# Kernel optimization log

Hardware: AMD Instinct MI355X
Metric: run time of the kernel (lower is better)

Reference implementation:

```python
import jax, jax.numpy as jnp
import numpy as np
import math

N_HEAD = 12

def alibi_slopes(h):
    x = (2 ** 8) ** (1.0 / h)
    return jnp.array([1.0 / x ** (i + 1) for i in range(h)], dtype=jnp.float32)

def setup_inputs() -> dict:
    key = jax.random.key(0)
    k0, k1, k2 = jax.random.split(key, 3)
    B, T, C = 4, 2048, 576
    x = jax.random.normal(k0, (B, T, C), dtype=jnp.float32)
    w_qkv = jax.random.normal(k1, (3 * C, C), dtype=jnp.float32) * 0.02
    w_proj = jax.random.normal(k2, (C, C), dtype=jnp.float32) * 0.02
    return {"x": x, "w_qkv": w_qkv, "w_proj": w_proj}

def reference(x, w_qkv, w_proj):
    B, T, C = x.shape
    H = N_HEAD
    D = C // H
    qkv = x @ w_qkv.T  # [B,T,3C]
    q, k, v = jnp.split(qkv, 3, axis=2)
    q = q.reshape(B, T, H, D).transpose(0, 2, 1, 3)  # [B,H,T,D]
    k = k.reshape(B, T, H, D).transpose(0, 2, 1, 3)
    v = v.reshape(B, T, H, D).transpose(0, 2, 1, 3)
    # value residual with v1=None: v = 0.5*v + 0.5*v = v (faithful no-op)
    scale = 1.0 / math.sqrt(D)
    att = jnp.einsum('bhid,bhjd->bhij', q, k) * scale  # [B,H,T,T]
    # ALiBi bias as written: (col - row).clamp(min=0) * slope (zero on causal part)
    col = jnp.arange(T, dtype=jnp.float32)[None, :]
    row = jnp.arange(T, dtype=jnp.float32)[:, None]
    bias = jnp.maximum(col - row, 0.0)[None, :, :] * alibi_slopes(H)[:, None, None]  # [H,T,T]
    att = att + bias[None]
    causal = (jnp.arange(T)[None, :] <= jnp.arange(T)[:, None])  # [T,T] lower-tri
    att = jnp.where(causal[None, None], att, -jnp.inf)
    att = jax.nn.softmax(att, axis=-1)
    y = jnp.einsum('bhij,bhjd->bhid', att, v)  # [B,H,T,D]
    y = y.transpose(0, 2, 1, 3).reshape(B, T, C)
    return y @ w_proj.T
```

## Files before the change

### kernel.cpp

```cpp
#include <hip/hip_runtime.h>
#include <math.h>

#define Bn 4
#define Tn 2048
#define Cn 576
#define Hn 12
#define Dn 48
#define Mn (Bn*Tn)

#define QSCALE (1.4426950408889634f * 0.14433756729740643f)

typedef short  short8  __attribute__((ext_vector_type(8)));
typedef float  floatx4 __attribute__((ext_vector_type(4)));
typedef unsigned short ushort_t;
typedef unsigned short ushort8_t __attribute__((ext_vector_type(8)));

static __device__ __forceinline__ unsigned short f2bf(float f) {
    union { float f; unsigned int u; } v; v.f = f;
    unsigned int r = v.u + 0x7FFFu + ((v.u >> 16) & 1u);
    return (unsigned short)(r >> 16);
}

static __device__ __forceinline__ unsigned int pack_trunc(float a, float b) {
    union { float f; unsigned int u; } ua, ub; ua.f = a; ub.f = b;
    return (ua.u >> 16) | (ub.u & 0xFFFF0000u);
}

static __device__ __forceinline__ void gload16(void* lds, const void* g) {
    __builtin_amdgcn_global_load_lds(
        (const __attribute__((address_space(1))) void*)g,
        (__attribute__((address_space(3))) void*)lds, 16, 0, 0);
}

__global__ __launch_bounds__(256)
void cast3(const float* __restrict__ a, ushort_t* __restrict__ oa, int na4,
           const float* __restrict__ b, ushort_t* __restrict__ ob, int nb4,
           const float* __restrict__ c, ushort_t* __restrict__ oc, int nc4)
{
    int i = blockIdx.x * 256 + threadIdx.x;
    const float* src; ushort_t* dst; int idx;
    if (i < na4)                  { src = a; dst = oa; idx = i; }
    else if (i < na4 + nb4)       { src = b; dst = ob; idx = i - na4; }
    else if (i < na4 + nb4 + nc4) { src = c; dst = oc; idx = i - na4 - nb4; }
    else return;
    float4 v = ((const float4*)src)[idx];
    ushort4 o;
    o.x = f2bf(v.x); o.y = f2bf(v.y); o.z = f2bf(v.z); o.w = f2bf(v.w);
    ((ushort4*)dst)[idx] = o;
}

template<int MODE, int MTILE>
__global__ __launch_bounds__(256)
void gemm_mfma(const ushort_t* __restrict__ A, const ushort_t* __restrict__ W,
               ushort_t* __restrict__ outb, float* __restrict__ outf)
{
    constexpr int SA   = MTILE / 16;
    constexpr int NSEG = SA + 4;
    constexpr int PW   = NSEG / 4;
    constexpr int MF   = MTILE / 64;
    constexpr int NB   = (MODE == 0) ? 27 : 9;
    __shared__ __align__(16) ushort_t Ls[2][NSEG][512];

    const int tid  = threadIdx.x;
    const int wave = tid >> 6;
    const int lane = tid & 63;
    const int m    = lane & 15;
    const int g    = lane >> 4;
    const int bid  = blockIdx.x;
    const int xcd  = bid & 7;
    const int slot = bid >> 3;
    const int n0   = (slot % NB) * 64;
    const int m0   = (xcd + 8 * (slot / NB)) * MTILE;

    floatx4 acc[MF][4];
    #pragma unroll
    for (int i = 0; i < MF; ++i)
        #pragma unroll
        for (int j = 0; j < 4; ++j)
            acc[i][j] = (floatx4){0.f, 0.f, 0.f, 0.f};

    const char* gp[PW];
    int         si[PW];
    #pragma unroll
    for (int i = 0; i < PW; ++i) {
        int s = wave + i * 4;
        si[i] = s;
        gp[i] = (s < SA)
            ? (const char*)(A + (size_t)(m0 + s * 16 + m) * Cn + g * 8)
            : (const char*)(W + (size_t)(n0 + (s - SA) * 16 + m) * Cn + g * 8);
    }

    #pragma unroll
    for (int i = 0; i < PW; ++i) { gload16(&Ls[0][si[i]][0], gp[i]); gp[i] += 64; }
    __syncthreads();

    int buf = 0;
    for (int k0 = 0; k0 < Cn; k0 += 32) {
        if (k0 + 32 < Cn) {
            #pragma unroll
            for (int i = 0; i < PW; ++i) { gload16(&Ls[buf ^ 1][si[i]][0], gp[i]); gp[i] += 64; }
        }
        short8 bf4[4];
        #pragma unroll
        for (int j = 0; j < 4; ++j) bf4[j] = *(const short8*)&Ls[buf][SA + j][lane * 8];
        #pragma unroll
        for (int i = 0; i < MF; ++i) {
            short8 af = *(const short8*)&Ls[buf][wave * MF + i][lane * 8];
            #pragma unroll
            for (int j = 0; j < 4; ++j)
                acc[i][j] = __builtin_amdgcn_mfma_f32_16x16x32_bf16(af, bf4[j], acc[i][j], 0, 0, 0);
        }
        __syncthreads();
        buf ^= 1;
    }

    const size_t per = (size_t)Bn * Hn * Tn * Dn;
    if (MODE == 0) {
        const int which = n0 / Cn;
        const int nb    = n0 - which * Cn;
        const int b     = m0 >> 11;
        const int t0g   = m0 & 2047;
        ushort_t* Lc = (ushort_t*)&Ls[0][0][0];
        if (which == 2) {
            constexpr int RS = MTILE + 8;
            #pragma unroll
            for (int i = 0; i < MF; ++i)
                #pragma unroll
                for (int j = 0; j < 4; ++j) {
                    ushort4 pk;
                    pk.x = f2bf(acc[i][j][0]); pk.y = f2bf(acc[i][j][1]);
                    pk.z = f2bf(acc[i][j][2]); pk.w = f2bf(acc[i][j][3]);
                    *(ushort4*)&Lc[(j * 16 + m) * RS + wave * (MTILE / 4) + i * 16 + g * 4] = pk;
                }
            __syncthreads();
            constexpr int CPC = MTILE / 8;
            constexpr int NIT = 64 * CPC / 256;
            #pragma unroll
            for (int it = 0; it < NIT; ++it) {
                int c    = tid + it * 256;
                int col  = c / CPC;
                int rowc = (c - col * CPC) * 8;
                int n    = nb + col;
                int h    = n / 48;
                int d    = n - h * 48;
                ushort_t* dst = outb + 2 * per
                    + (((size_t)(b * Hn + h) * Dn + d) * Tn) + t0g + rowc;
                *(ushort8_t*)dst = *(const ushort8_t*)&Lc[col * RS + rowc];
            }
        } else {
            const float sc = (which == 0) ? QSCALE : 1.0f;
            #pragma unroll
            for (int i = 0; i < MF; ++i)
                #pragma unroll
                for (int j = 0; j < 4; ++j)
                    #pragma unroll
                    for (int r = 0; r < 4; ++r)
                        Lc[(wave * (MTILE / 4) + i * 16 + g * 4 + r) * 80 + j * 16 + m] =
                            f2bf(acc[i][j][r] * sc);
            __syncthreads();
            constexpr int NIT = MTILE * 8 / 256;
            #pragma unroll
            for (int it = 0; it < NIT; ++it) {
                int c   = tid + it * 256;
                int row = c >> 3;
                int c8  = (c & 7) * 8;
                int n   = nb + c8;
                int h   = n / 48;
                int d   = n - h * 48;
                ushort_t* dst = outb + (size_t)which * per
                    + (((size_t)(b * Hn + h) * Tn + t0g + row) * Dn) + d;
                *(ushort8_t*)dst = *(const ushort8_t*)&Lc[row * 80 + c8];
            }
        }
    } else {
        #pragma unroll
        for (int i = 0; i < MF; ++i) {
            #pragma unroll
            for (int r = 0; r < 4; ++r) {
                int mrow = m0 + wave * (MTILE / 4) + i * 16 + g * 4 + r;
                #pragma unroll
                for (int j = 0; j < 4; ++j)
                    outf[(size_t)mrow * Cn + n0 + j * 16 + m] = acc[i][j][r];
            }
        }
    }
}

__global__ __launch_bounds__(512, 6)
void attn_mfma(const ushort_t* __restrict__ Q, const ushort_t* __restrict__ K,
               const ushort_t* __restrict__ V, ushort_t* __restrict__ Y,
               const ushort_t* __restrict__ zb)
{
    __shared__ __align__(16) ushort_t QPs[16][512];
    __shared__ __align__(16) ushort_t Ks[2][8][512];
    __shared__ __align__(16) ushort_t Vs[2][6][512];

    const int id   = blockIdx.x;
    const int kk   = id / 48;
    const int bh   = id - kk * 48;
    const int QT   = (kk & 1) ? (kk >> 1) : (15 - (kk >> 1));
    const int tid  = threadIdx.x;
    const int wave = tid >> 6;
    const int lane = tid & 63;
    const int m    = lane & 15;
    const int g    = lane >> 4;
    const int q0   = QT * 128;
    const int nkt  = 2 * QT + 2;

    const ushort_t* Qp = Q + (size_t)bh * Tn * Dn;
    const ushort_t* Kp = K + (size_t)bh * Tn * Dn;
    const ushort_t* Vp = V + (size_t)bh * Dn * Tn;

    {
        const char* qrp = (const char*)(Qp + (size_t)(q0 + wave * 16 + m) * Dn);
        gload16(&QPs[wave * 2 + 0][0], qrp + g * 16);
        gload16(&QPs[wave * 2 + 1][0], (g < 2) ? (qrp + 64 + g * 16) : (const char*)zb);
    }

    const bool  kpad = ((wave & 1) == 1) && (g >= 2);
    const char* kptr = kpad ? (const char*)zb
        : (const char*)(Kp + (size_t)((wave >> 1) * 16 + m) * Dn) + (wave & 1) * 64 + g * 16;
    const int   kadv = kpad ? 0 : 64 * Dn * 2;
    const char* vptr = (const char*)(Vp + (size_t)((wave >> 1) * 16 + m) * Tn)
                       + (wave & 1) * 64 + g * 16;
    const int   vadv = 64 * 2;

    gload16(&Ks[0][wave][0], kptr); kptr += kadv;
    if (wave < 6) { gload16(&Vs[0][wave][0], vptr); vptr += vadv; }
    __syncthreads();

    short8 bq[2];
    bq[0] = *(const short8*)&QPs[wave * 2 + 0][lane * 8];
    bq[1] = *(const short8*)&QPs[wave * 2 + 1][lane * 8];

    floatx4 acc[3];
    #pragma unroll
    for (int t = 0; t < 3; ++t) acc[t] = (floatx4){0.f, 0.f, 0.f, 0.f};
    float l_tot = 0.f;
    const int qrow  = q0 + wave * 16 + m;
    const int qwmin = q0 + wave * 16;
    const int qwmax = qwmin + 15;

    for (int jt = 0; jt < nkt; ++jt) {
        const int cur = jt & 1;
        const int j0  = jt * 64;
        if (jt + 1 < nkt) {
            gload16(&Ks[cur ^ 1][wave][0], kptr); kptr += kadv;
            if (wave < 6) { gload16(&Vs[cur ^ 1][wave][0], vptr); vptr += vadv; }
        }

        if (j0 <= qwmax) {
            floatx4 s[4];
            #pragma unroll
            for (int t = 0; t < 4; ++t) {
                s[t] = (floatx4){0.f, 0.f, 0.f, 0.f};
                #pragma unroll
                for (int kc = 0; kc < 2; ++kc) {
                    short8 ak = *(const short8*)&Ks[cur][t * 2 + kc][lane * 8];
                    s[t] = __builtin_amdgcn_mfma_f32_16x16x32_bf16(ak, bq[kc], s[t], 0, 0, 0);
                }
            }

            float p[4][4];
            float lsum = 0.f;
            if (j0 + 63 > qwmin) {
                #pragma unroll
                for (int t = 0; t < 4; ++t)
                    #pragma unroll
                    for (int r = 0; r < 4; ++r) {
                        int j = j0 + t * 16 + g * 4 + r;
                        float v = (j <= qrow) ? s[t][r] : -1e30f;
                        float e = __builtin_amdgcn_exp2f(v);
                        p[t][r] = e; lsum += e;
                    }
            } else {
                #pragma unroll
                for (int t = 0; t < 4; ++t)
                    #pragma unroll
                    for (int r = 0; r < 4; ++r) {
                        float e = __builtin_amdgcn_exp2f(s[t][r]);
                        p[t][r] = e; lsum += e;
                    }
            }
            lsum += __shfl_xor(lsum, 16);
            lsum += __shfl_xor(lsum, 32);
            l_tot += lsum;

            #pragma unroll
            for (int t = 0; t < 4; ++t) {
                uint2 w2;
                w2.x = pack_trunc(p[t][0], p[t][1]);
                w2.y = pack_trunc(p[t][2], p[t][3]);
                *(uint2*)&QPs[wave * 2 + (t >> 1)]
                             [(2 * (t & 1) + (g >> 1)) * 128 + m * 8 + (g & 1) * 4] = w2;
            }
            asm volatile("s_waitcnt lgkmcnt(0)" ::: "memory");

            #pragma unroll
            for (int kc = 0; kc < 2; ++kc) {
                short8 bp = *(const short8*)&QPs[wave * 2 + kc][lane * 8];
                #pragma unroll
                for (int t = 0; t < 3; ++t) {
                    short8 av = *(const short8*)&Vs[cur][t * 2 + kc][lane * 8];
                    acc[t] = __builtin_amdgcn_mfma_f32_16x16x32_bf16(av, bp, acc[t], 0, 0, 0);
                }
            }
        }

        __syncthreads();
    }

    const float inv = 1.0f / l_tot;
    const int b = bh / Hn;
    const int h = bh - b * Hn;
    ushort_t* yp = Y + ((size_t)(b * Tn + qrow)) * Cn + h * Dn;
    #pragma unroll
    for (int t = 0; t < 3; ++t) {
        ushort4 o;
        o.x = f2bf(acc[t][0] * inv);
        o.y = f2bf(acc[t][1] * inv);
        o.z = f2bf(acc[t][2] * inv);
        o.w = f2bf(acc[t][3] * inv);
        *(ushort4*)&yp[t * 16 + g * 4] = o;
    }
}

extern "C" void kernel_launch(void* const* d_in, const int* in_sizes, int n_in,
                              void* d_out, int out_size, void* d_ws, size_t ws_size,
                              hipStream_t stream)
{
    const float* x      = (const float*)d_in[0];
    const float* w_qkv  = (const float*)d_in[1];
    const float* w_proj = (const float*)d_in[2];
    float* out = (float*)d_out;

    const size_t per = (size_t)Bn * Hn * Tn * Dn;

    ushort_t* xb  = (ushort_t*)d_ws;
    ushort_t* wqb = xb  + (size_t)Mn * Cn;
    ushort_t* wpb = wqb + (size_t)3 * Cn * Cn;
    ushort_t* qkv = wpb + (size_t)Cn * Cn;
    ushort_t* yb  = qkv + 3 * per;
    ushort_t* zb  = yb  + (size_t)Mn * Cn;

    hipMemsetAsync(zb, 0, 256, stream);

    const int na4 = Mn * Cn / 4, nb4 = 3 * Cn * Cn / 4, nc4 = Cn * Cn / 4;
    cast3<<<dim3((na4 + nb4 + nc4 + 255) / 256), dim3(256), 0, stream>>>(
        x, xb, na4, w_qkv, wqb, nb4, w_proj, wpb, nc4);

    gemm_mfma<0, 256><<<dim3((Mn / 256) * 27), dim3(256), 0, stream>>>(xb, wqb, qkv, nullptr);

    attn_mfma<<<dim3((Tn / 128) * Bn * Hn), dim3(512), 0, stream>>>(
        qkv, qkv + per, qkv + 2 * per, yb, zb);

    gemm_mfma<1, 128><<<dim3((Mn / 128) * 9), dim3(256), 0, stream>>>(yb, wpb, nullptr, out);
}
```

Before: 185.8 us.

## Deepen GEMM K-loop pipeline to four LDS buffers with three stages in flight

Replaces the double-buffered global-to-LDS prefetch in the bf16 MFMA GEMM with a 4-buffer ring that keeps three K-stages in flight. Partial s_waitcnt vmcnt waits plus raw s_barrier replace __syncthreads, so outstanding loads for later stages are not drained every iteration. The aim is to hide global load latency behind MFMA work, at the cost of twice the LDS footprint, which may reduce occupancy. The hand-coded vmcnt immediates must match the number of loads issued per wave.

```diff
diff --git a/kernel.cpp b/kernel.cpp
--- a/kernel.cpp
+++ b/kernel.cpp
@@ -30,6 +30,21 @@
     __builtin_amdgcn_global_load_lds(
         (const __attribute__((address_space(1))) void*)g,
         (__attribute__((address_space(3))) void*)lds, 16, 0, 0);
+}
+
+template<int N> static __device__ __forceinline__ void wait_vm_lg() {
+    if constexpr (N == 0)
+        asm volatile("s_waitcnt vmcnt(0) lgkmcnt(0)" ::: "memory");
+    else if constexpr (N == 3)
+        asm volatile("s_waitcnt vmcnt(3) lgkmcnt(0)" ::: "memory");
+    else if constexpr (N == 5)
+        asm volatile("s_waitcnt vmcnt(5) lgkmcnt(0)" ::: "memory");
+    else if constexpr (N == 6)
+        asm volatile("s_waitcnt vmcnt(6) lgkmcnt(0)" ::: "memory");
+    else if constexpr (N == 10)
+        asm volatile("s_waitcnt vmcnt(10) lgkmcnt(0)" ::: "memory");
+    else
+        static_assert(N == -12345, "unsupported waitcnt immediate");
 }
 
 __global__ __launch_bounds__(256)
@@ -59,7 +74,10 @@
     constexpr int PW   = NSEG / 4;
     constexpr int MF   = MTILE / 64;
     constexpr int NB   = (MODE == 0) ? 27 : 9;
-    __shared__ __align__(16) ushort_t Ls[2][NSEG][512];
+    constexpr int NST  = Cn / 32;
+    constexpr int AH   = 3;
+    constexpr int NBUF = 4;
+    __shared__ __align__(16) ushort_t Ls[NBUF][NSEG][512];
 
     const int tid  = threadIdx.x;
     const int wave = tid >> 6;
@@ -91,27 +109,36 @@
     }
 
     #pragma unroll
-    for (int i = 0; i < PW; ++i) { gload16(&Ls[0][si[i]][0], gp[i]); gp[i] += 64; }
-    __syncthreads();
-
-    int buf = 0;
-    for (int k0 = 0; k0 < Cn; k0 += 32) {
-        if (k0 + 32 < Cn) {
-            #pragma unroll
-            for (int i = 0; i < PW; ++i) { gload16(&Ls[buf ^ 1][si[i]][0], gp[i]); gp[i] += 64; }
-        }
+    for (int s = 0; s < AH; ++s)
+        #pragma unroll
+        for (int i = 0; i < PW; ++i) { gload16(&Ls[s][si[i]][0], gp[i]); gp[i] += 64; }
+    wait_vm_lg<(AH - 1) * PW>();
+    __builtin_amdgcn_s_barrier();
+
+    for (int j = 0; j < NST; ++j) {
+        if (j + AH < NST) {
+            #pragma unroll
+            for (int i = 0; i < PW; ++i) {
+                gload16(&Ls[(j + AH) & (NBUF - 1)][si[i]][0], gp[i]);
+                gp[i] += 64;
+            }
+        }
+        const int buf = j & (NBUF - 1);
         short8 bf4[4];
         #pragma unroll
-        for (int j = 0; j < 4; ++j) bf4[j] = *(const short8*)&Ls[buf][SA + j][lane * 8];
+        for (int jj = 0; jj < 4; ++jj)
+            bf4[jj] = *(const short8*)&Ls[buf][SA + jj][lane * 8];
         #pragma unroll
         for (int i = 0; i < MF; ++i) {
             short8 af = *(const short8*)&Ls[buf][wave * MF + i][lane * 8];
             #pragma unroll
-            for (int j = 0; j < 4; ++j)
-                acc[i][j] = __builtin_amdgcn_mfma_f32_16x16x32_bf16(af, bf4[j], acc[i][j], 0, 0, 0);
-        }
-        __syncthreads();
-        buf ^= 1;
+            for (int jj = 0; jj < 4; ++jj)
+                acc[i][jj] = __builtin_amdgcn_mfma_f32_16x16x32_bf16(af, bf4[jj], acc[i][jj], 0, 0, 0);
+        }
+        if (j < NST - AH)        wait_vm_lg<(AH - 1) * PW>();
+        else if (j == NST - AH)  wait_vm_lg<(AH - 2) * PW>();
+        else                     wait_vm_lg<0>();
+        __builtin_amdgcn_s_barrier();
     }
 
     const size_t per = (size_t)Bn * Hn * Tn * Dn;
```

New measurement: 183.9 us. About the same (-1.0%).

## Replace LDS-staged GEMMs with large-tile direct-register MFMA GEMMs and fold memset

Applied to the files above, without the earlier changes.

Both the QKV and output projection GEMMs are rewritten. They now load A and W fragments straight from global memory into registers, with no LDS double buffering. Tiles are larger (256x256 for QKV, 128x192 for proj), 8 waves per block, and grids are sized near one block per CU. The zero-buffer memset is folded into the cast kernel to drop a launch. The goal is to cut LDS traffic, barriers and launch overhead, at the cost of uncoalesced global fragment loads, higher register pressure, and fewer blocks to hide latency.

```diff
diff --git a/kernel.cpp b/kernel.cpp
--- a/kernel.cpp
+++ b/kernel.cpp
@@ -35,9 +35,14 @@
 __global__ __launch_bounds__(256)
 void cast3(const float* __restrict__ a, ushort_t* __restrict__ oa, int na4,
            const float* __restrict__ b, ushort_t* __restrict__ ob, int nb4,
-           const float* __restrict__ c, ushort_t* __restrict__ oc, int nc4)
+           const float* __restrict__ c, ushort_t* __restrict__ oc, int nc4,
+           ushort_t* __restrict__ zb)
 {
     int i = blockIdx.x * 256 + threadIdx.x;
+    if (blockIdx.x == 0 && threadIdx.x < 16) {
+        float4 z = (float4){0.f, 0.f, 0.f, 0.f};
+        ((float4*)zb)[threadIdx.x] = z;
+    }
     const float* src; ushort_t* dst; int idx;
     if (i < na4)                  { src = a; dst = oa; idx = i; }
     else if (i < na4 + nb4)       { src = b; dst = ob; idx = i - na4; }
@@ -49,139 +54,183 @@
     ((ushort4*)dst)[idx] = o;
 }
 
-template<int MODE, int MTILE>
-__global__ __launch_bounds__(256)
-void gemm_mfma(const ushort_t* __restrict__ A, const ushort_t* __restrict__ W,
-               ushort_t* __restrict__ outb, float* __restrict__ outf)
+__global__ __launch_bounds__(512)
+void gemm_qkv(const ushort_t* __restrict__ A, const ushort_t* __restrict__ W,
+              ushort_t* __restrict__ outb)
 {
-    constexpr int SA   = MTILE / 16;
-    constexpr int NSEG = SA + 4;
-    constexpr int PW   = NSEG / 4;
-    constexpr int MF   = MTILE / 64;
-    constexpr int NB   = (MODE == 0) ? 27 : 9;
-    __shared__ __align__(16) ushort_t Ls[2][NSEG][512];
+    __shared__ __align__(16) ushort_t Lc[34816];
 
     const int tid  = threadIdx.x;
     const int wave = tid >> 6;
     const int lane = tid & 63;
     const int m    = lane & 15;
     const int g    = lane >> 4;
+    const int wr   = wave >> 2;
+    const int wn   = wave & 3;
+
     const int bid  = blockIdx.x;
     const int xcd  = bid & 7;
     const int slot = bid >> 3;
-    const int n0   = (slot % NB) * 64;
-    const int m0   = (xcd + 8 * (slot / NB)) * MTILE;
-
-    floatx4 acc[MF][4];
-    #pragma unroll
-    for (int i = 0; i < MF; ++i)
+    const int ng   = slot % 7;
+    const int mg   = xcd + 8 * (slot / 7);
+    const int m0   = mg * 256;
+    const int n0g  = ng * 256;
+
+    const ushort_t* Ab = A + (size_t)(m0  + wr * 128 + m) * Cn + g * 8;
+    const ushort_t* Wb = W + (size_t)(n0g + wn * 64  + m) * Cn + g * 8;
+
+    floatx4 acc[8][4];
+    #pragma unroll
+    for (int i = 0; i < 8; ++i)
         #pragma unroll
         for (int j = 0; j < 4; ++j)
             acc[i][j] = (floatx4){0.f, 0.f, 0.f, 0.f};
 
-    const char* gp[PW];
-    int         si[PW];
-    #pragma unroll
-    for (int i = 0; i < PW; ++i) {
-        int s = wave + i * 4;
-        si[i] = s;
-        gp[i] = (s < SA)
-            ? (const char*)(A + (size_t)(m0 + s * 16 + m) * Cn + g * 8)
-            : (const char*)(W + (size_t)(n0 + (s - SA) * 16 + m) * Cn + g * 8);
-    }
-
-    #pragma unroll
-    for (int i = 0; i < PW; ++i) { gload16(&Ls[0][si[i]][0], gp[i]); gp[i] += 64; }
+    #pragma unroll 2
+    for (int h = 0; h < 18; ++h) {
+        short8 af[8], bf[4];
+        #pragma unroll
+        for (int mf = 0; mf < 8; ++mf)
+            af[mf] = *(const short8*)(Ab + (size_t)mf * 16 * Cn + h * 32);
+        #pragma unroll
+        for (int nf = 0; nf < 4; ++nf)
+            bf[nf] = *(const short8*)(Wb + (size_t)nf * 16 * Cn + h * 32);
+        #pragma unroll
+        for (int mf = 0; mf < 8; ++mf)
+            #pragma unroll
+            for (int nf = 0; nf < 4; ++nf)
+                acc[mf][nf] = __builtin_amdgcn_mfma_f32_16x16x32_bf16(
+                    af[mf], bf[nf], acc[mf][nf], 0, 0, 0);
+    }
+
+    const size_t per = (size_t)Bn * Hn * Tn * Dn;
+    const int b  = m0 >> 11;
+    const int t0 = m0 & 2047;
+
     __syncthreads();
 
-    int buf = 0;
-    for (int k0 = 0; k0 < Cn; k0 += 32) {
-        if (k0 + 32 < Cn) {
-            #pragma unroll
-            for (int i = 0; i < PW; ++i) { gload16(&Ls[buf ^ 1][si[i]][0], gp[i]); gp[i] += 64; }
-        }
-        short8 bf4[4];
-        #pragma unroll
-        for (int j = 0; j < 4; ++j) bf4[j] = *(const short8*)&Ls[buf][SA + j][lane * 8];
-        #pragma unroll
-        for (int i = 0; i < MF; ++i) {
-            short8 af = *(const short8*)&Ls[buf][wave * MF + i][lane * 8];
-            #pragma unroll
-            for (int j = 0; j < 4; ++j)
-                acc[i][j] = __builtin_amdgcn_mfma_f32_16x16x32_bf16(af, bf4[j], acc[i][j], 0, 0, 0);
+    #pragma unroll
+    for (int h2 = 0; h2 < 2; ++h2) {
+        const int  nbase = n0g + h2 * 128;
+        const bool vmode = (nbase >= 1152);
+        if ((wn >> 1) == h2) {
+            if (!vmode) {
+                #pragma unroll
+                for (int mf = 0; mf < 8; ++mf)
+                    #pragma unroll
+                    for (int nf = 0; nf < 4; ++nf) {
+                        const int  nfb = n0g + wn * 64 + nf * 16;
+                        const float sc = (nfb < 576) ? QSCALE : 1.0f;
+                        const int col = (wn & 1) * 64 + nf * 16 + m;
+                        const int rb  = wr * 128 + mf * 16 + g * 4;
+                        #pragma unroll
+                        for (int r = 0; r < 4; ++r)
+                            Lc[(rb + r) * 136 + col] = f2bf(acc[mf][nf][r] * sc);
+                    }
+            } else {
+                #pragma unroll
+                for (int mf = 0; mf < 8; ++mf)
+                    #pragma unroll
+                    for (int nf = 0; nf < 4; ++nf) {
+                        const int col = (wn & 1) * 64 + nf * 16 + m;
+                        const int rb  = wr * 128 + mf * 16 + g * 4;
+                        ushort4 pk;
+                        pk.x = f2bf(acc[mf][nf][0]); pk.y = f2bf(acc[mf][nf][1]);
+                        pk.z = f2bf(acc[mf][nf][2]); pk.w = f2bf(acc[mf][nf][3]);
+                        *(ushort4*)&Lc[col * 264 + rb] = pk;
+                    }
+            }
         }
         __syncthreads();
-        buf ^= 1;
-    }
-
-    const size_t per = (size_t)Bn * Hn * Tn * Dn;
-    if (MODE == 0) {
-        const int which = n0 / Cn;
-        const int nb    = n0 - which * Cn;
-        const int b     = m0 >> 11;
-        const int t0g   = m0 & 2047;
-        ushort_t* Lc = (ushort_t*)&Ls[0][0][0];
-        if (which == 2) {
-            constexpr int RS = MTILE + 8;
-            #pragma unroll
-            for (int i = 0; i < MF; ++i)
-                #pragma unroll
-                for (int j = 0; j < 4; ++j) {
-                    ushort4 pk;
-                    pk.x = f2bf(acc[i][j][0]); pk.y = f2bf(acc[i][j][1]);
-                    pk.z = f2bf(acc[i][j][2]); pk.w = f2bf(acc[i][j][3]);
-                    *(ushort4*)&Lc[(j * 16 + m) * RS + wave * (MTILE / 4) + i * 16 + g * 4] = pk;
+        if (!vmode) {
+            #pragma unroll
+            for (int it = 0; it < 8; ++it) {
+                const int c   = tid + it * 512;
+                const int row = c >> 4;
+                const int c8  = (c & 15) * 8;
+                const int n   = nbase + c8;
+                const int which = (n >= 576);
+                const int nn  = n - which * 576;
+                const int h   = nn / 48, d = nn - h * 48;
+                ushort_t* dst = outb + (size_t)which * per
+                    + ((size_t)(b * Hn + h) * Tn + t0 + row) * Dn + d;
+                *(ushort8_t*)dst = *(const ushort8_t*)&Lc[row * 136 + c8];
+            }
+        } else {
+            #pragma unroll
+            for (int it = 0; it < 8; ++it) {
+                const int c   = tid + it * 512;
+                const int col = c >> 5;
+                const int rc  = (c & 31) * 8;
+                const int n   = nbase + col;
+                if (n < 1728) {
+                    const int dd = n - 1152;
+                    const int h  = dd / 48, d = dd - h * 48;
+                    ushort_t* dst = outb + 2 * per
+                        + ((size_t)(b * Hn + h) * Dn + d) * Tn + t0 + rc;
+                    *(ushort8_t*)dst = *(const ushort8_t*)&Lc[col * 264 + rc];
                 }
-            __syncthreads();
-            constexpr int CPC = MTILE / 8;
-            constexpr int NIT = 64 * CPC / 256;
-            #pragma unroll
-            for (int it = 0; it < NIT; ++it) {
-                int c    = tid + it * 256;
-                int col  = c / CPC;
-                int rowc = (c - col * CPC) * 8;
-                int n    = nb + col;
-                int h    = n / 48;
-                int d    = n - h * 48;
-                ushort_t* dst = outb + 2 * per
-                    + (((size_t)(b * Hn + h) * Dn + d) * Tn) + t0g + rowc;
-                *(ushort8_t*)dst = *(const ushort8_t*)&Lc[col * RS + rowc];
-            }
-        } else {
-            const float sc = (which == 0) ? QSCALE : 1.0f;
-            #pragma unroll
-            for (int i = 0; i < MF; ++i)
-                #pragma unroll
-                for (int j = 0; j < 4; ++j)
-                    #pragma unroll
-                    for (int r = 0; r < 4; ++r)
-                        Lc[(wave * (MTILE / 4) + i * 16 + g * 4 + r) * 80 + j * 16 + m] =
-                            f2bf(acc[i][j][r] * sc);
-            __syncthreads();
-            constexpr int NIT = MTILE * 8 / 256;
-            #pragma unroll
-            for (int it = 0; it < NIT; ++it) {
-                int c   = tid + it * 256;
-                int row = c >> 3;
-                int c8  = (c & 7) * 8;
-                int n   = nb + c8;
-                int h   = n / 48;
-                int d   = n - h * 48;
-                ushort_t* dst = outb + (size_t)which * per
-                    + (((size_t)(b * Hn + h) * Tn + t0g + row) * Dn) + d;
-                *(ushort8_t*)dst = *(const ushort8_t*)&Lc[row * 80 + c8];
             }
         }
-    } else {
-        #pragma unroll
-        for (int i = 0; i < MF; ++i) {
-            #pragma unroll
-            for (int r = 0; r < 4; ++r) {
-                int mrow = m0 + wave * (MTILE / 4) + i * 16 + g * 4 + r;
-                #pragma unroll
-                for (int j = 0; j < 4; ++j)
-                    outf[(size_t)mrow * Cn + n0 + j * 16 + m] = acc[i][j][r];
-            }
+        __syncthreads();
+    }
+}
+
+__global__ __launch_bounds__(512)
+void gemm_proj(const ushort_t* __restrict__ A, const ushort_t* __restrict__ W,
+               float* __restrict__ outf)
+{
+    const int tid  = threadIdx.x;
+    const int wave = tid >> 6;
+    const int lane = tid & 63;
+    const int m    = lane & 15;
+    const int g    = lane >> 4;
+    const int wr   = wave >> 2;
+    const int wn   = wave & 3;
+
+    const int bid  = blockIdx.x;
+    const int xcd  = bid & 7;
+    const int slot = bid >> 3;
+    const int ng   = slot % 3;
+    const int mg   = xcd + 8 * (slot / 3);
+    const int m0   = mg * 128;
+    const int n0   = ng * 192 + wn * 48;
+
+    const ushort_t* Ab = A + (size_t)(m0 + wr * 64 + m) * Cn + g * 8;
+    const ushort_t* Wb = W + (size_t)(n0 + m) * Cn + g * 8;
+
+    floatx4 acc[4][3];
+    #pragma unroll
+    for (int i = 0; i < 4; ++i)
+        #pragma unroll
+        for (int j = 0; j < 3; ++j)
+            acc[i][j] = (floatx4){0.f, 0.f, 0.f, 0.f};
+
+    #pragma unroll 2
+    for (int h = 0; h < 18; ++h) {
+        short8 af[4], bf[3];
+        #pragma unroll
+        for (int mf = 0; mf < 4; ++mf)
+            af[mf] = *(const short8*)(Ab + (size_t)mf * 16 * Cn + h * 32);
+        #pragma unroll
+        for (int nf = 0; nf < 3; ++nf)
+            bf[nf] = *(const short8*)(Wb + (size_t)nf * 16 * Cn + h * 32);
+        #pragma unroll
+        for (int mf = 0; mf < 4; ++mf)
+            #pragma unroll
+            for (int nf = 0; nf < 3; ++nf)
+                acc[mf][nf] = __builtin_amdgcn_mfma_f32_16x16x32_bf16(
+                    af[mf], bf[nf], acc[mf][nf], 0, 0, 0);
+    }
+
+    #pragma unroll
+    for (int mf = 0; mf < 4; ++mf) {
+        #pragma unroll
+        for (int r = 0; r < 4; ++r) {
+            const int mrow = m0 + wr * 64 + mf * 16 + g * 4 + r;
+            #pragma unroll
+            for (int nf = 0; nf < 3; ++nf)
+                outf[(size_t)mrow * Cn + n0 + nf * 16 + m] = acc[mf][nf][r];
         }
     }
 }
@@ -343,16 +392,14 @@
     ushort_t* yb  = qkv + 3 * per;
     ushort_t* zb  = yb  + (size_t)Mn * Cn;
 
-    hipMemsetAsync(zb, 0, 256, stream);
-
     const int na4 = Mn * Cn / 4, nb4 = 3 * Cn * Cn / 4, nc4 = Cn * Cn / 4;
     cast3<<<dim3((na4 + nb4 + nc4 + 255) / 256), dim3(256), 0, stream>>>(
-        x, xb, na4, w_qkv, wqb, nb4, w_proj, wpb, nc4);
-
-    gemm_mfma<0, 256><<<dim3((Mn / 256) * 27), dim3(256), 0, stream>>>(xb, wqb, qkv, nullptr);
+        x, xb, na4, w_qkv, wqb, nb4, w_proj, wpb, nc4, zb);
+
+    gemm_qkv<<<dim3(224), dim3(512), 0, stream>>>(xb, wqb, qkv);
 
     attn_mfma<<<dim3((Tn / 128) * Bn * Hn), dim3(512), 0, stream>>>(
         qkv, qkv + per, qkv + 2 * per, yb, zb);
 
-    gemm_mfma<1, 128><<<dim3((Mn / 128) * 9), dim3(256), 0, stream>>>(yb, wpb, nullptr, out);
-}
+    gemm_proj<<<dim3(192), dim3(512), 0, stream>>>(yb, wpb, out);
+}
```

After: 205.3 us. 1.1x slower.
